# Performance work log

Measured on AMD Instinct MI355X. Metric: run time of the kernel, lower is better.

## Reference

```python
import jax, jax.numpy as jnp
import numpy as np

# --- constants mirroring consts.* in the torch module ---
B = 4          # batch (consts.batch_sz)
DK = 256       # key/query channels
DV = 516       # value channels = 4*batch_sz*len_of_lookup + 4
HS, WS = 64, 64  # H//8, W//8 for H=W=512
L_MEM = 32     # consts.L (lookup length / buffer truncation)
M_BUF = 32     # pre-existing buffer entries
LOG_BASE = 2.0 # consts.N used as log base
ALPHA = 0.5    # module sets alpha=0 (degenerate); use 0.5 so attention path is exercised


def _xavier_uniform(key, shape):
    fan_in, fan_out = shape[0], shape[1]
    a = np.sqrt(6.0 / (fan_in + fan_out)).astype(np.float32)
    return jax.random.uniform(key, shape, jnp.float32, -a, a)


def setup_inputs() -> dict:
    key = jax.random.key(0)
    ks = jax.random.split(key, 7)
    return {
        "fc": jax.random.normal(ks[0], (B, DK, HS, WS), jnp.float32),
        "fm": jax.random.normal(ks[1], (B, DV, HS, WS), jnp.float32),
        "key_buffer": jax.random.normal(ks[2], (M_BUF, DK, HS, WS), jnp.float32),
        "value_buffer": jax.random.normal(ks[3], (M_BUF, DV, HS, WS), jnp.float32),
        "Q": _xavier_uniform(ks[4], (DK, DK)),
        "K": _xavier_uniform(ks[5], (DK, DK)),
        "V": _xavier_uniform(ks[6], (DV, DV)),
    }


def reference(fc, fm, key_buffer, value_buffer, Q, K, V):
    # channel projection per spatial location: 'ijkl,jm->imkl'
    q = jnp.einsum('bchw,cd->bdhw', fc, Q)            # [B, DK, h, w]
    k_new = jnp.einsum('bchw,cd->bdhw', fc, K)        # [B, DK, h, w]
    v_new = jnp.einsum('bchw,cd->bdhw', fm, V)        # [B, DV, h, w]

    # KV-buffer append (new entries first, matching cat(new, buffer)), then
    # truncate to the most recent L_MEM entries (current_batch >= L branch)
    k = jnp.concatenate([k_new, key_buffer], axis=0)[-L_MEM:]   # [L, DK, h, w]
    v = jnp.concatenate([v_new, value_buffer], axis=0)[-L_MEM:] # [L, DV, h, w]

    # non-standard temperature: log_N(L*h*w + h*w) / sqrt(DK)
    h, w = fc.shape[2], fc.shape[3]
    temp = np.float32(np.log(L_MEM * h * w + h * w) / np.log(LOG_BASE) / np.sqrt(DK))

    # per-pixel attention over memory entries ('ijkl,mjkl->imkl')
    scores = temp * jnp.einsum('ichw,mchw->imhw', q, k)  # [B, L, h, w]
    attn = jax.nn.softmax(scores, axis=1)                # softmax over memory dim
    out = jnp.einsum('imhw,mchw->ichw', attn, v)         # [B, DV, h, w]

    return fm + ALPHA * out
```

## Files before the change

### kernel.cpp

```cpp
#include <hip/hip_runtime.h>
#include <math.h>

#define HW   4096
#define DKC  256
#define DVC  516
#define LM   32
#define NB   4
#define P1   8

__device__ __forceinline__ int xcd_swizzle(int bid, int nwg) {
    int chunk = nwg >> 3;
    return (bid & 7) * chunk + (bid >> 3);
}

__global__ __launch_bounds__(256) void k_attn(const float* __restrict__ fc,
                                              const float* __restrict__ Qw,
                                              const float* __restrict__ kbuf,
                                              float* __restrict__ attn,
                                              float temp) {
    __shared__ float smem[8192 + 1024];
    float* sc_t = smem + 8192;
    const int t   = threadIdx.x;
    const int px0 = xcd_swizzle(blockIdx.x, gridDim.x) * P1;

    #pragma unroll
    for (int i = 0; i < 32; ++i) {
        int f  = i * 256 + t;
        int b  = f >> 11;
        int c  = (f >> 3) & 255;
        int px = f & 7;
        smem[c * 32 + px * 4 + b] = fc[(b * DKC + c) * HW + px0 + px];
    }
    __syncthreads();

    const int px   = t & 7;
    const int dgrp = t >> 3;
    const int d0   = dgrp * 8;
    float acc[4][8];
    #pragma unroll
    for (int b = 0; b < 4; ++b)
        #pragma unroll
        for (int i = 0; i < 8; ++i) acc[b][i] = 0.0f;

    for (int c = 0; c < 256; ++c) {
        float4 fcv = *(const float4*)&smem[c * 32 + px * 4];
        float4 q0  = *(const float4*)&Qw[c * 256 + d0];
        float4 q1  = *(const float4*)&Qw[c * 256 + d0 + 4];
        float fq[8] = {q0.x, q0.y, q0.z, q0.w, q1.x, q1.y, q1.z, q1.w};
        float fb[4] = {fcv.x, fcv.y, fcv.z, fcv.w};
        #pragma unroll
        for (int b = 0; b < 4; ++b)
            #pragma unroll
            for (int i = 0; i < 8; ++i)
                acc[b][i] += fb[b] * fq[i];
    }
    __syncthreads();

    #pragma unroll
    for (int b = 0; b < 4; ++b) {
        *(float4*)&smem[(b * 8 + px) * 256 + d0]     = make_float4(acc[b][0], acc[b][1], acc[b][2], acc[b][3]);
        *(float4*)&smem[(b * 8 + px) * 256 + d0 + 4] = make_float4(acc[b][4], acc[b][5], acc[b][6], acc[b][7]);
    }
    __syncthreads();

    const int m = t >> 3;
    float s[4] = {0.f, 0.f, 0.f, 0.f};
    for (int d = 0; d < 256; d += 4) {
        float kv0 = kbuf[(m * DKC + d + 0) * HW + px0 + px];
        float kv1 = kbuf[(m * DKC + d + 1) * HW + px0 + px];
        float kv2 = kbuf[(m * DKC + d + 2) * HW + px0 + px];
        float kv3 = kbuf[(m * DKC + d + 3) * HW + px0 + px];
        #pragma unroll
        for (int b = 0; b < 4; ++b) {
            float4 qv = *(const float4*)&smem[(b * 8 + px) * 256 + d];
            s[b] += qv.x * kv0 + qv.y * kv1 + qv.z * kv2 + qv.w * kv3;
        }
    }
    #pragma unroll
    for (int b = 0; b < 4; ++b) sc_t[(b * 32 + m) * 8 + px] = s[b] * temp;
    __syncthreads();

    if (t < 32) {
        int b = t >> 3, p = t & 7;
        float mx = -1e30f;
        for (int mm = 0; mm < 32; ++mm) mx = fmaxf(mx, sc_t[(b * 32 + mm) * 8 + p]);
        float sum = 0.f;
        for (int mm = 0; mm < 32; ++mm) sum += expf(sc_t[(b * 32 + mm) * 8 + p] - mx);
        float inv = 1.0f / sum;
        for (int mm = 0; mm < 32; ++mm)
            attn[(b * 32 + mm) * HW + px0 + p] = expf(sc_t[(b * 32 + mm) * 8 + p] - mx) * inv;
    }
}

__global__ __launch_bounds__(256) void k_out(const float* __restrict__ vbuf,
                                             const float* __restrict__ fm,
                                             const float* __restrict__ attn,
                                             float* __restrict__ out) {
    __shared__ float a_lds[4 * 32 * 64];
    const int t   = threadIdx.x;
    const int sw  = xcd_swizzle(blockIdx.x, gridDim.x);
    const int px0 = (sw & 63) * 64;
    const int c0  = (sw >> 6) * 12;

    #pragma unroll
    for (int i = 0; i < 32; ++i) {
        int f  = i * 256 + t;
        int b  = f >> 11;
        int m  = (f >> 6) & 31;
        int px = f & 63;
        a_lds[f] = attn[(b * 32 + m) * HW + px0 + px];
    }
    __syncthreads();

    const int px   = t & 63;
    const int cidx = t >> 6;
    float acc[4][3] = {};
    for (int m = 0; m < 32; ++m) {
        float a0 = a_lds[(0 * 32 + m) * 64 + px];
        float a1 = a_lds[(1 * 32 + m) * 64 + px];
        float a2 = a_lds[(2 * 32 + m) * 64 + px];
        float a3 = a_lds[(3 * 32 + m) * 64 + px];
        #pragma unroll
        for (int j = 0; j < 3; ++j) {
            int c = c0 + cidx * 3 + j;
            float vv = vbuf[(m * DVC + c) * HW + px0 + px];
            acc[0][j] += a0 * vv;
            acc[1][j] += a1 * vv;
            acc[2][j] += a2 * vv;
            acc[3][j] += a3 * vv;
        }
    }
    #pragma unroll
    for (int j = 0; j < 3; ++j) {
        int c = c0 + cidx * 3 + j;
        #pragma unroll
        for (int b = 0; b < 4; ++b) {
            int idx = (b * DVC + c) * HW + px0 + px;
            out[idx] = fm[idx] + 0.5f * acc[b][j];
        }
    }
}

extern "C" void kernel_launch(void* const* d_in, const int* in_sizes, int n_in,
                              void* d_out, int out_size, void* d_ws, size_t ws_size,
                              hipStream_t stream) {
    const float* fc = (const float*)d_in[0];
    const float* fm = (const float*)d_in[1];
    const float* kb = (const float*)d_in[2];
    const float* vb = (const float*)d_in[3];
    const float* Qw = (const float*)d_in[4];
    float* out  = (float*)d_out;
    float* attn = (float*)d_ws;

    const float temp = (float)(log(32.0 * 4096.0 + 4096.0) / log(2.0) / 16.0);

    k_attn<<<HW / P1, 256, 0, stream>>>(fc, Qw, kb, attn, temp);
    k_out<<<64 * (DVC / 12), 256, 0, stream>>>(vb, fm, attn, out);
}
```

Baseline: 551.4 us.

## Fuse attention and value-aggregation kernels, keeping softmax weights in LDS

Merges the score/softmax kernel and the value-weighting kernel into one launch. Softmax weights stay in shared memory rather than going through a global workspace, and each 8-pixel block now computes all 516 output channels, 16 per thread plus a 4-channel tail. This removes a kernel launch and the global write and re-read of the attention weights. In exchange, value-buffer reads become narrow 8-pixel segments spread across many rows, only 512 blocks carry the dominant V stream, and each thread holds 64 accumulators, which raises register pressure.

```diff
diff --git a/kernel.cpp b/kernel.cpp
--- a/kernel.cpp
+++ b/kernel.cpp
@@ -13,11 +13,13 @@
     return (bid & 7) * chunk + (bid >> 3);
 }
 
-__global__ __launch_bounds__(256) void k_attn(const float* __restrict__ fc,
-                                              const float* __restrict__ Qw,
-                                              const float* __restrict__ kbuf,
-                                              float* __restrict__ attn,
-                                              float temp) {
+__global__ __launch_bounds__(256) void k_fused(const float* __restrict__ fc,
+                                               const float* __restrict__ Qw,
+                                               const float* __restrict__ kbuf,
+                                               const float* __restrict__ vbuf,
+                                               const float* __restrict__ fm,
+                                               float* __restrict__ out,
+                                               float temp) {
     __shared__ float smem[8192 + 1024];
     float* sc_t = smem + 8192;
     const int t   = threadIdx.x;
@@ -88,55 +90,56 @@
         for (int mm = 0; mm < 32; ++mm) sum += expf(sc_t[(b * 32 + mm) * 8 + p] - mx);
         float inv = 1.0f / sum;
         for (int mm = 0; mm < 32; ++mm)
-            attn[(b * 32 + mm) * HW + px0 + p] = expf(sc_t[(b * 32 + mm) * 8 + p] - mx) * inv;
-    }
-}
-
-__global__ __launch_bounds__(256) void k_out(const float* __restrict__ vbuf,
-                                             const float* __restrict__ fm,
-                                             const float* __restrict__ attn,
-                                             float* __restrict__ out) {
-    __shared__ float a_lds[4 * 32 * 64];
-    const int t   = threadIdx.x;
-    const int sw  = xcd_swizzle(blockIdx.x, gridDim.x);
-    const int px0 = (sw & 63) * 64;
-    const int c0  = (sw >> 6) * 12;
-
-    #pragma unroll
-    for (int i = 0; i < 32; ++i) {
-        int f  = i * 256 + t;
-        int b  = f >> 11;
-        int m  = (f >> 6) & 31;
-        int px = f & 63;
-        a_lds[f] = attn[(b * 32 + m) * HW + px0 + px];
+            sc_t[(b * 32 + mm) * 8 + p] = expf(sc_t[(b * 32 + mm) * 8 + p] - mx) * inv;
     }
     __syncthreads();
 
-    const int px   = t & 63;
-    const int cidx = t >> 6;
-    float acc[4][3] = {};
-    for (int m = 0; m < 32; ++m) {
-        float a0 = a_lds[(0 * 32 + m) * 64 + px];
-        float a1 = a_lds[(1 * 32 + m) * 64 + px];
-        float a2 = a_lds[(2 * 32 + m) * 64 + px];
-        float a3 = a_lds[(3 * 32 + m) * 64 + px];
+    const int cg = t >> 3;
+    float va[4][16];
+    #pragma unroll
+    for (int b = 0; b < 4; ++b)
         #pragma unroll
-        for (int j = 0; j < 3; ++j) {
-            int c = c0 + cidx * 3 + j;
-            float vv = vbuf[(m * DVC + c) * HW + px0 + px];
-            acc[0][j] += a0 * vv;
-            acc[1][j] += a1 * vv;
-            acc[2][j] += a2 * vv;
-            acc[3][j] += a3 * vv;
+        for (int j = 0; j < 16; ++j) va[b][j] = 0.0f;
+
+    for (int mm = 0; mm < 32; ++mm) {
+        float a0 = sc_t[(0 * 32 + mm) * 8 + px];
+        float a1 = sc_t[(1 * 32 + mm) * 8 + px];
+        float a2 = sc_t[(2 * 32 + mm) * 8 + px];
+        float a3 = sc_t[(3 * 32 + mm) * 8 + px];
+        const float* vrow = &vbuf[(mm * DVC + cg * 16) * HW + px0 + px];
+        #pragma unroll
+        for (int j = 0; j < 16; ++j) {
+            float vv = vrow[j * HW];
+            va[0][j] += a0 * vv;
+            va[1][j] += a1 * vv;
+            va[2][j] += a2 * vv;
+            va[3][j] += a3 * vv;
         }
     }
     #pragma unroll
-    for (int j = 0; j < 3; ++j) {
-        int c = c0 + cidx * 3 + j;
+    for (int j = 0; j < 16; ++j) {
+        int c = cg * 16 + j;
         #pragma unroll
         for (int b = 0; b < 4; ++b) {
             int idx = (b * DVC + c) * HW + px0 + px;
-            out[idx] = fm[idx] + 0.5f * acc[b][j];
+            out[idx] = fm[idx] + 0.5f * va[b][j];
+        }
+    }
+
+    if (cg < 4) {
+        int c = 512 + cg;
+        float vt[4] = {0.f, 0.f, 0.f, 0.f};
+        for (int mm = 0; mm < 32; ++mm) {
+            float vv = vbuf[(mm * DVC + c) * HW + px0 + px];
+            vt[0] += sc_t[(0 * 32 + mm) * 8 + px] * vv;
+            vt[1] += sc_t[(1 * 32 + mm) * 8 + px] * vv;
+            vt[2] += sc_t[(2 * 32 + mm) * 8 + px] * vv;
+            vt[3] += sc_t[(3 * 32 + mm) * 8 + px] * vv;
+        }
+        #pragma unroll
+        for (int b = 0; b < 4; ++b) {
+            int idx = (b * DVC + c) * HW + px0 + px;
+            out[idx] = fm[idx] + 0.5f * vt[b];
         }
     }
 }
@@ -150,10 +153,9 @@
     const float* vb = (const float*)d_in[3];
     const float* Qw = (const float*)d_in[4];
     float* out  = (float*)d_out;
-    float* attn = (float*)d_ws;
+    (void)d_ws; (void)ws_size;
 
     const float temp = (float)(log(32.0 * 4096.0 + 4096.0) / log(2.0) / 16.0);
 
-    k_attn<<<HW / P1, 256, 0, stream>>>(fc, Qw, kb, attn, temp);
-    k_out<<<64 * (DVC / 12), 256, 0, stream>>>(vb, fm, attn, out);
+    k_fused<<<HW / P1, 256, 0, stream>>>(fc, Qw, kb, vb, fm, out, temp);
 }
```

Measured after the change: 577.8 us. 1.05x slower.
